# Performance work log

Measured on AMD Instinct MI355X. Metric: run time of the kernel, lower is better.

Reference implementation:

```python
import jax, jax.numpy as jnp
import numpy as np

N = 40000
E = 640000
DIN = 128
H = 128
G = 16
C = 10


def setup_inputs() -> dict:
    key = jax.random.key(0)
    ks = jax.random.split(key, 12)
    x = jax.random.normal(ks[0], (N, DIN), dtype=jnp.float32)
    edge_index = jax.random.randint(ks[1], (2, E), 0, N, dtype=jnp.int64)
    batch = jnp.sort(jax.random.randint(ks[2], (N,), 0, G, dtype=jnp.int64))
    s = 1.0 / np.sqrt(H)
    W_in = jax.random.normal(ks[3], (DIN, H), dtype=jnp.float32) * s
    b_in = jnp.zeros((H,), dtype=jnp.float32)
    W1 = jax.random.normal(ks[4], (H, H), dtype=jnp.float32) * s
    b1 = jnp.zeros((H,), dtype=jnp.float32)
    W2 = jax.random.normal(ks[5], (H, H), dtype=jnp.float32) * s
    b2 = jnp.zeros((H,), dtype=jnp.float32)
    Wf1 = jax.random.normal(ks[6], (H, H // 2), dtype=jnp.float32) * s
    bf1 = jnp.zeros((H // 2,), dtype=jnp.float32)
    Wf2 = jax.random.normal(ks[7], (H // 2, C), dtype=jnp.float32) * (1.0 / np.sqrt(H // 2))
    bf2 = jnp.zeros((C,), dtype=jnp.float32)
    return {"x": x, "edge_index": edge_index, "batch": batch,
            "W_in": W_in, "b_in": b_in, "W1": W1, "b1": b1,
            "W2": W2, "b2": b2, "Wf1": Wf1, "bf1": bf1,
            "Wf2": Wf2, "bf2": bf2}


def _gcn_conv(h, src, dst, deg_inv_sqrt, W, b):
    # h' = D^{-1/2} (A + I) D^{-1/2} (h W) + b  (PyG GCNConv with self-loops)
    hw = h @ W  # [N, H]
    norm = deg_inv_sqrt[src] * deg_inv_sqrt[dst]  # [E]
    agg = jax.ops.segment_sum(hw[src] * norm[:, None], dst, num_segments=N)
    agg = agg + hw * (deg_inv_sqrt * deg_inv_sqrt)[:, None]  # self-loop term
    return agg + b


def reference(x, edge_index, batch, W_in, b_in, W1, b1, W2, b2, Wf1, bf1, Wf2, bf2):
    src, dst = edge_index[0], edge_index[1]
    # degree on target nodes, including self-loop (+1)
    deg = jax.ops.segment_sum(jnp.ones((E,), dtype=x.dtype), dst, num_segments=N) + 1.0
    deg_inv_sqrt = jax.lax.rsqrt(deg)

    h = x @ W_in + b_in
    h = jax.nn.relu(_gcn_conv(h, src, dst, deg_inv_sqrt, W1, b1))  # dropout is identity in eval
    h = jax.nn.relu(_gcn_conv(h, src, dst, deg_inv_sqrt, W2, b2))

    # global mean pool by graph id
    sums = jax.ops.segment_sum(h, batch, num_segments=G)  # [G, H]
    counts = jax.ops.segment_sum(jnp.ones((N,), dtype=h.dtype), batch, num_segments=G)
    pooled = sums / jnp.maximum(counts, 1.0)[:, None]

    out = jax.nn.relu(pooled @ Wf1 + bf1) @ Wf2 + bf2  # [G, C]
    return out
```

## Files before the change

kernel.cpp:

```cpp
#include <hip/hip_runtime.h>

#define NN 40000
#define EE 640000
#define NCH 157

typedef unsigned int uint;
typedef unsigned short ushort;
typedef __attribute__((ext_vector_type(8))) short short8;
typedef __attribute__((ext_vector_type(4))) float floatx4;

__device__ inline ushort f2bf(float f) {
    uint u = __float_as_uint(f);
    return (ushort)((u + 0x7fffu + ((u >> 16) & 1u)) >> 16);
}
__device__ inline float bf_lo(uint u) { return __uint_as_float(u << 16); }
__device__ inline float bf_hi(uint u) { return __uint_as_float(u & 0xffff0000u); }

__device__ inline int lower_bound_dev(const int* __restrict__ a, int n, int x) {
    int lo = 0, hi = n;
    while (lo < hi) { int m = (lo + hi) >> 1; if (a[m] < x) lo = m + 1; else hi = m; }
    return lo;
}

__global__ __launch_bounds__(256) void histprep_kernel(const int* __restrict__ dst,
                                                       int* __restrict__ counts,
                                                       const float* __restrict__ W_in,
                                                       const float* __restrict__ W1,
                                                       const float* __restrict__ b_in,
                                                       const float* __restrict__ W2,
                                                       const int* __restrict__ batch,
                                                       ushort* __restrict__ Bp1,
                                                       ushort* __restrict__ Bp2,
                                                       float* __restrict__ cvec,
                                                       int* __restrict__ glo) {
    int b = blockIdx.x, t = threadIdx.x;
    if (b < 2500) {
        atomicAdd(&counts[dst[b * 256 + t]], 1);
    } else if (b < 2564) {
        int idx = (b - 2500) * 256 + t;
        int k = idx >> 7, n = idx & 127;
        float s = 0.f;
        for (int j = 0; j < 128; ++j) s = fmaf(W_in[k * 128 + j], W1[j * 128 + n], s);
        Bp1[((size_t)(k >> 3) * 128 + n) * 8 + (k & 7)] = f2bf(s);
    } else if (b < 2628) {
        int idx = (b - 2564) * 256 + t;
        int k = idx >> 7, n = idx & 127;
        Bp2[((size_t)(k >> 3) * 128 + n) * 8 + (k & 7)] = f2bf(W2[idx]);
    } else {
        if (t < 128) {
            float s = 0.f;
            for (int k = 0; k < 128; ++k) s = fmaf(b_in[k], W1[k * 128 + t], s);
            cvec[t] = s;
        } else if (t < 128 + 17) {
            int g = t - 128;
            glo[g] = lower_bound_dev(batch, NN, g);
        }
    }
}

__global__ __launch_bounds__(256) void scan_kernel(const int* __restrict__ counts,
                                                   int* __restrict__ goff,
                                                   int* __restrict__ start,
                                                   int* __restrict__ cursor,
                                                   float* __restrict__ dis, int N) {
    __shared__ int ws[4];
    __shared__ int sbase;
    int t = threadIdx.x, lane = t & 63, wv = t >> 6;
    int idx = blockIdx.x * 256 + t;
    int c = (idx < N) ? counts[idx] : 0;
    int v = c;
    #pragma unroll
    for (int d = 1; d < 64; d <<= 1) {
        int u = __shfl_up(v, d, 64);
        if (lane >= d) v += u;
    }
    if (lane == 63) ws[wv] = v;
    __syncthreads();
    if (t == 0) {
        int total = ws[0] + ws[1] + ws[2] + ws[3];
        sbase = atomicAdd(goff, total);
    }
    __syncthreads();
    int off = sbase;
    for (int j = 0; j < wv; ++j) off += ws[j];
    if (idx < N) {
        int excl = off + v - c;
        start[idx] = excl;
        cursor[idx] = excl;
        dis[idx] = rsqrtf((float)c + 1.0f);
    }
}

template <bool ABF16>
__device__ inline void mm_tile(const void* __restrict__ Av, const ushort* __restrict__ Bpack,
                               ushort* __restrict__ C, int tile, int wv, int lane) {
    int m = lane & 15, q = lane >> 4;
    int row = tile * 64 + wv * 16 + m;

    short8 afr[4];
    if (ABF16) {
        const ushort* A = (const ushort*)Av;
        const ushort* ap = A + (size_t)row * 128 + q * 8;
        #pragma unroll
        for (int k0 = 0; k0 < 4; ++k0) afr[k0] = *(const short8*)(ap + k0 * 32);
    } else {
        const float* A = (const float*)Av;
        const float* ap = A + (size_t)row * 128 + q * 8;
        #pragma unroll
        for (int k0 = 0; k0 < 4; ++k0) {
            float4 f0 = *(const float4*)(ap + k0 * 32);
            float4 f1 = *(const float4*)(ap + k0 * 32 + 4);
            short8 a;
            a[0] = (short)f2bf(f0.x); a[1] = (short)f2bf(f0.y);
            a[2] = (short)f2bf(f0.z); a[3] = (short)f2bf(f0.w);
            a[4] = (short)f2bf(f1.x); a[5] = (short)f2bf(f1.y);
            a[6] = (short)f2bf(f1.z); a[7] = (short)f2bf(f1.w);
            afr[k0] = a;
        }
    }

    floatx4 acc[8];
    #pragma unroll
    for (int nt = 0; nt < 8; ++nt) { floatx4 z = {0.f, 0.f, 0.f, 0.f}; acc[nt] = z; }

    #pragma unroll
    for (int nt = 0; nt < 8; ++nt) {
        #pragma unroll
        for (int k0 = 0; k0 < 4; ++k0) {
            short8 bfrag = *(const short8*)(Bpack + ((size_t)(k0 * 4 + q) * 128 + nt * 16 + m) * 8);
            acc[nt] = __builtin_amdgcn_mfma_f32_16x16x32_bf16(afr[k0], bfrag, acc[nt], 0, 0, 0);
        }
    }

    int orow_base = tile * 64 + wv * 16 + q * 4;
    #pragma unroll
    for (int nt = 0; nt < 8; ++nt) {
        #pragma unroll
        for (int r = 0; r < 4; ++r)
            C[(size_t)(orow_base + r) * 128 + nt * 16 + m] = f2bf(acc[nt][r]);
    }
}

__global__ __launch_bounds__(256) void fillmm1_kernel(const int* __restrict__ src,
                                                      const int* __restrict__ dst,
                                                      const float* __restrict__ dis,
                                                      int* __restrict__ cursor,
                                                      int2* __restrict__ edata,
                                                      const float* __restrict__ x,
                                                      const ushort* __restrict__ Bp1,
                                                      ushort* __restrict__ bufA) {
    int b = blockIdx.x, t = threadIdx.x;
    if (b < 2500) {
        int e = b * 256 + t;
        int s = src[e], d = dst[e];
        int pos = atomicAdd(&cursor[d], 1);
        float nrm = dis[s] * dis[d];
        int2 v; v.x = s; v.y = __float_as_int(nrm);
        edata[pos] = v;
    } else {
        mm_tile<false>(x, Bp1, bufA, b - 2500, t >> 6, t & 63);
    }
}

__global__ __launch_bounds__(256) void mm2_kernel(const ushort* __restrict__ A,
                                                  const ushort* __restrict__ Bp2,
                                                  ushort* __restrict__ C) {
    mm_tile<true>(A, Bp2, C, blockIdx.x, threadIdx.x >> 6, threadIdx.x & 63);
}

__global__ __launch_bounds__(256) void agg_kernel(const ushort* __restrict__ hw,
                                                  const float* __restrict__ dis,
                                                  const int* __restrict__ start,
                                                  const int* __restrict__ counts,
                                                  const int2* __restrict__ edata,
                                                  const float* __restrict__ cvec,
                                                  const float* __restrict__ bias,
                                                  ushort* __restrict__ out, int N) {
    __shared__ int2 eds[4][64];
    int wv = threadIdx.x >> 6;
    int lane = threadIdx.x & 63;
    int i = blockIdx.x * 4 + wv;
    if (i >= N) return;
    int beg = start[i];
    int deg = counts[i];
    int dmain = deg > 64 ? 64 : deg;
    const uint* __restrict__ hv = (const uint*)hw;

    int2 ed;
    if (lane < dmain) ed = edata[beg + lane];
    else { ed.x = i; ed.y = 0; }
    eds[wv][lane] = ed;

    float di = dis[i];
    float sii = di * di;
    uint su = hv[(size_t)i * 64 + lane];
    float a0 = sii * bf_lo(su);
    float a1 = sii * bf_hi(su);
    float sumnorm = sii;

    int dpad = (dmain + 7) & ~7;
    for (int j = 0; j < dpad; j += 8) {
        int2 e0 = eds[wv][j],     e1 = eds[wv][j + 1];
        int2 e2 = eds[wv][j + 2], e3 = eds[wv][j + 3];
        int2 e4 = eds[wv][j + 4], e5 = eds[wv][j + 5];
        int2 e6 = eds[wv][j + 6], e7 = eds[wv][j + 7];
        uint u0 = hv[(size_t)e0.x * 64 + lane];
        uint u1 = hv[(size_t)e1.x * 64 + lane];
        uint u2 = hv[(size_t)e2.x * 64 + lane];
        uint u3 = hv[(size_t)e3.x * 64 + lane];
        uint u4 = hv[(size_t)e4.x * 64 + lane];
        uint u5 = hv[(size_t)e5.x * 64 + lane];
        uint u6 = hv[(size_t)e6.x * 64 + lane];
        uint u7 = hv[(size_t)e7.x * 64 + lane];
        float n0 = __int_as_float(e0.y), n1 = __int_as_float(e1.y);
        float n2 = __int_as_float(e2.y), n3 = __int_as_float(e3.y);
        float n4 = __int_as_float(e4.y), n5 = __int_as_float(e5.y);
        float n6 = __int_as_float(e6.y), n7 = __int_as_float(e7.y);
        a0 = fmaf(n0, bf_lo(u0), a0); a1 = fmaf(n0, bf_hi(u0), a1);
        a0 = fmaf(n1, bf_lo(u1), a0); a1 = fmaf(n1, bf_hi(u1), a1);
        a0 = fmaf(n2, bf_lo(u2), a0); a1 = fmaf(n2, bf_hi(u2), a1);
        a0 = fmaf(n3, bf_lo(u3), a0); a1 = fmaf(n3, bf_hi(u3), a1);
        a0 = fmaf(n4, bf_lo(u4), a0); a1 = fmaf(n4, bf_hi(u4), a1);
        a0 = fmaf(n5, bf_lo(u5), a0); a1 = fmaf(n5, bf_hi(u5), a1);
        a0 = fmaf(n6, bf_lo(u6), a0); a1 = fmaf(n6, bf_hi(u6), a1);
        a0 = fmaf(n7, bf_lo(u7), a0); a1 = fmaf(n7, bf_hi(u7), a1);
        sumnorm += ((n0 + n1) + (n2 + n3)) + ((n4 + n5) + (n6 + n7));
    }
    for (int e = beg + 64; e < beg + deg; ++e) {
        int2 et = edata[e];
        float n0 = __int_as_float(et.y);
        uint u0 = hv[(size_t)et.x * 64 + lane];
        a0 = fmaf(n0, bf_lo(u0), a0);
        a1 = fmaf(n0, bf_hi(u0), a1);
        sumnorm += n0;
    }

    float c0 = 0.f, c1 = 0.f;
    if (cvec) { c0 = cvec[2 * lane]; c1 = cvec[2 * lane + 1]; }
    float b0 = bias[2 * lane], b1 = bias[2 * lane + 1];
    float o0 = fmaxf(fmaf(sumnorm, c0, a0) + b0, 0.f);
    float o1 = fmaxf(fmaf(sumnorm, c1, a1) + b1, 0.f);
    uint o = (uint)f2bf(o0) | ((uint)f2bf(o1) << 16);
    ((uint*)out)[(size_t)i * 64 + lane] = o;
}

__global__ __launch_bounds__(256) void poolfinal_kernel(const ushort* __restrict__ h,
                                                        const int* __restrict__ glo,
                                                        float* __restrict__ pools,
                                                        int* __restrict__ ticket,
                                                        const float* __restrict__ Wf1,
                                                        const float* __restrict__ bf1,
                                                        const float* __restrict__ Wf2,
                                                        const float* __restrict__ bf2,
                                                        float* __restrict__ out) {
    __shared__ float pooled[16][128];
    __shared__ float z[16][64];
    __shared__ int slast;
    int t = threadIdx.x, c2 = t & 63, wv = t >> 6;
    int b = blockIdx.x;
    int g = b >> 3, ch = b & 7;
    int lo = glo[g], hi = glo[g + 1];
    int span = hi - lo;
    int chunk = (span + 7) >> 3;
    int r0 = lo + ch * chunk;
    int r1 = hi < r0 + chunk ? hi : r0 + chunk;
    const uint* __restrict__ hv = (const uint*)h;

    float a0 = 0.f, a1 = 0.f;
    #pragma unroll 4
    for (int j = r0 + wv; j < r1; j += 4) {
        uint u = hv[(size_t)j * 64 + c2];
        a0 += bf_lo(u);
        a1 += bf_hi(u);
    }
    if (r0 < r1) {
        atomicAdd(&pools[g * 128 + 2 * c2], a0);
        atomicAdd(&pools[g * 128 + 2 * c2 + 1], a1);
    }

    __syncthreads();
    __threadfence();
    if (t == 0) slast = atomicAdd(ticket, 1);
    __syncthreads();
    if (slast != 127) return;

    for (int idx = t; idx < 2048; idx += 256) {
        int gg = idx >> 7, c = idx & 127;
        int cn = glo[gg + 1] - glo[gg];
        float cnf = (float)(cn > 1 ? cn : 1);
        float ps = __hip_atomic_load(&pools[idx], __ATOMIC_RELAXED, __HIP_MEMORY_SCOPE_AGENT);
        pooled[gg][c] = ps / cnf;
    }
    __syncthreads();
    for (int idx = t; idx < 1024; idx += 256) {
        int gg = idx >> 6, j = idx & 63;
        float s = bf1[j];
        for (int k = 0; k < 128; ++k) s = fmaf(pooled[gg][k], Wf1[k * 64 + j], s);
        z[gg][j] = fmaxf(s, 0.f);
    }
    __syncthreads();
    if (t < 160) {
        int gg = t / 10, k = t % 10;
        float s = bf2[k];
        for (int j = 0; j < 64; ++j) s = fmaf(z[gg][j], Wf2[j * 10 + k], s);
        out[t] = s;
    }
}


extern "C" void kernel_launch(void* const* d_in, const int* in_sizes, int n_in,
                              void* d_out, int out_size, void* d_ws, size_t ws_size,
                              hipStream_t stream) {
    const float* x    = (const float*)d_in[0];
    const int* edge   = (const int*)d_in[1];
    const int* batch  = (const int*)d_in[2];
    const float* W_in = (const float*)d_in[3];
    const float* b_in = (const float*)d_in[4];
    const float* W1   = (const float*)d_in[5];
    const float* b1   = (const float*)d_in[6];
    const float* W2   = (const float*)d_in[7];
    const float* b2   = (const float*)d_in[8];
    const float* Wf1  = (const float*)d_in[9];
    const float* bf1  = (const float*)d_in[10];
    const float* Wf2  = (const float*)d_in[11];
    const float* bf2  = (const float*)d_in[12];
    float* out = (float*)d_out;

    char* ws = (char*)d_ws;
    size_t off = 0;
    auto alloc = [&](size_t bytes) -> void* {
        void* p = ws + off;
        off += (bytes + 511) & ~(size_t)511;
        return p;
    };
    int* counts   = (int*)alloc((size_t)NN * 4);
    float* pools  = (float*)alloc(16 * 128 * 4);
    int* misc     = (int*)alloc(512);
    size_t zero_bytes = off;
    int* goff     = misc;
    int* ticket   = misc + 1;
    int* glo      = misc + 8;
    ushort* bufA  = (ushort*)alloc((size_t)NN * 128 * 2);
    ushort* bufB  = (ushort*)alloc((size_t)NN * 128 * 2);
    ushort* Bp1   = (ushort*)alloc(128 * 128 * 2);
    ushort* Bp2   = (ushort*)alloc(128 * 128 * 2);
    float* cvec   = (float*)alloc(128 * 4);
    float* dis    = (float*)alloc((size_t)NN * 4);
    int* start    = (int*)alloc((size_t)NN * 4);
    int* cursor   = (int*)alloc((size_t)NN * 4);
    int2* edata   = (int2*)alloc((size_t)EE * 8);

    hipMemsetAsync(counts, 0, zero_bytes, stream);

    histprep_kernel<<<2629, 256, 0, stream>>>(edge + EE, counts, W_in, W1, b_in, W2,
                                              batch, Bp1, Bp2, cvec, glo);
    scan_kernel<<<NCH, 256, 0, stream>>>(counts, goff, start, cursor, dis, NN);
    fillmm1_kernel<<<2500 + NN / 64, 256, 0, stream>>>(edge, edge + EE, dis, cursor,
                                                       edata, x, Bp1, bufA);
    agg_kernel<<<NN / 4, 256, 0, stream>>>(bufA, dis, start, counts, edata, cvec, b1, bufB, NN);
    mm2_kernel<<<NN / 64, 256, 0, stream>>>(bufB, Bp2, bufA);
    agg_kernel<<<NN / 4, 256, 0, stream>>>(bufA, dis, start, counts, edata, nullptr, b2, bufB, NN);
    poolfinal_kernel<<<128, 256, 0, stream>>>(bufB, glo, pools, ticket,
                                              Wf1, bf1, Wf2, bf2, out);
}
```

Measured before the change: 240.5 us.

## Fuse first aggregation with second matmul and second aggregation with mean pooling

The first GCN aggregation now writes a 16-row tile into shared memory, and the same block multiplies it by W2 with MFMA, so the separate mm2 launch and its round trip of h1 through global memory go away. The second aggregation accumulates the pooled sums directly, reducing per block in shared memory when all 16 rows belong to one graph and using atomics otherwise. The last block, found by a ticket counter, runs the final MLP. This removes two kernel launches and two full-size intermediate writes and reads. In exchange each aggregation block has only 4 waves processing 4 nodes each serially, and the matmul tile is smaller, which may lower occupancy and weight reuse.

```diff
diff --git a/kernel.cpp b/kernel.cpp
--- a/kernel.cpp
+++ b/kernel.cpp
@@ -91,32 +91,23 @@
     }
 }
 
-template <bool ABF16>
-__device__ inline void mm_tile(const void* __restrict__ Av, const ushort* __restrict__ Bpack,
-                               ushort* __restrict__ C, int tile, int wv, int lane) {
+__device__ inline void mm_tile_f32(const float* __restrict__ A, const ushort* __restrict__ Bpack,
+                                   ushort* __restrict__ C, int tile, int wv, int lane) {
     int m = lane & 15, q = lane >> 4;
     int row = tile * 64 + wv * 16 + m;
 
     short8 afr[4];
-    if (ABF16) {
-        const ushort* A = (const ushort*)Av;
-        const ushort* ap = A + (size_t)row * 128 + q * 8;
-        #pragma unroll
-        for (int k0 = 0; k0 < 4; ++k0) afr[k0] = *(const short8*)(ap + k0 * 32);
-    } else {
-        const float* A = (const float*)Av;
-        const float* ap = A + (size_t)row * 128 + q * 8;
-        #pragma unroll
-        for (int k0 = 0; k0 < 4; ++k0) {
-            float4 f0 = *(const float4*)(ap + k0 * 32);
-            float4 f1 = *(const float4*)(ap + k0 * 32 + 4);
-            short8 a;
-            a[0] = (short)f2bf(f0.x); a[1] = (short)f2bf(f0.y);
-            a[2] = (short)f2bf(f0.z); a[3] = (short)f2bf(f0.w);
-            a[4] = (short)f2bf(f1.x); a[5] = (short)f2bf(f1.y);
-            a[6] = (short)f2bf(f1.z); a[7] = (short)f2bf(f1.w);
-            afr[k0] = a;
-        }
+    const float* ap = A + (size_t)row * 128 + q * 8;
+    #pragma unroll
+    for (int k0 = 0; k0 < 4; ++k0) {
+        float4 f0 = *(const float4*)(ap + k0 * 32);
+        float4 f1 = *(const float4*)(ap + k0 * 32 + 4);
+        short8 a;
+        a[0] = (short)f2bf(f0.x); a[1] = (short)f2bf(f0.y);
+        a[2] = (short)f2bf(f0.z); a[3] = (short)f2bf(f0.w);
+        a[4] = (short)f2bf(f1.x); a[5] = (short)f2bf(f1.y);
+        a[6] = (short)f2bf(f1.z); a[7] = (short)f2bf(f1.w);
+        afr[k0] = a;
     }
 
     floatx4 acc[8];
@@ -158,38 +149,23 @@
         int2 v; v.x = s; v.y = __float_as_int(nrm);
         edata[pos] = v;
     } else {
-        mm_tile<false>(x, Bp1, bufA, b - 2500, t >> 6, t & 63);
-    }
-}
-
-__global__ __launch_bounds__(256) void mm2_kernel(const ushort* __restrict__ A,
-                                                  const ushort* __restrict__ Bp2,
-                                                  ushort* __restrict__ C) {
-    mm_tile<true>(A, Bp2, C, blockIdx.x, threadIdx.x >> 6, threadIdx.x & 63);
-}
-
-__global__ __launch_bounds__(256) void agg_kernel(const ushort* __restrict__ hw,
-                                                  const float* __restrict__ dis,
-                                                  const int* __restrict__ start,
-                                                  const int* __restrict__ counts,
-                                                  const int2* __restrict__ edata,
-                                                  const float* __restrict__ cvec,
-                                                  const float* __restrict__ bias,
-                                                  ushort* __restrict__ out, int N) {
-    __shared__ int2 eds[4][64];
-    int wv = threadIdx.x >> 6;
-    int lane = threadIdx.x & 63;
-    int i = blockIdx.x * 4 + wv;
-    if (i >= N) return;
+        mm_tile_f32(x, Bp1, bufA, b - 2500, t >> 6, t & 63);
+    }
+}
+
+__device__ inline void agg_core(const uint* __restrict__ hv, const float* __restrict__ dis,
+                                const int* __restrict__ start, const int* __restrict__ counts,
+                                const int2* __restrict__ edata, const float* __restrict__ cvec,
+                                const float* __restrict__ bias, int i, int lane,
+                                int2* __restrict__ eds, float& o0, float& o1) {
     int beg = start[i];
     int deg = counts[i];
     int dmain = deg > 64 ? 64 : deg;
-    const uint* __restrict__ hv = (const uint*)hw;
 
     int2 ed;
     if (lane < dmain) ed = edata[beg + lane];
     else { ed.x = i; ed.y = 0; }
-    eds[wv][lane] = ed;
+    eds[lane] = ed;
 
     float di = dis[i];
     float sii = di * di;
@@ -200,10 +176,10 @@
 
     int dpad = (dmain + 7) & ~7;
     for (int j = 0; j < dpad; j += 8) {
-        int2 e0 = eds[wv][j],     e1 = eds[wv][j + 1];
-        int2 e2 = eds[wv][j + 2], e3 = eds[wv][j + 3];
-        int2 e4 = eds[wv][j + 4], e5 = eds[wv][j + 5];
-        int2 e6 = eds[wv][j + 6], e7 = eds[wv][j + 7];
+        int2 e0 = eds[j],     e1 = eds[j + 1];
+        int2 e2 = eds[j + 2], e3 = eds[j + 3];
+        int2 e4 = eds[j + 4], e5 = eds[j + 5];
+        int2 e6 = eds[j + 6], e7 = eds[j + 7];
         uint u0 = hv[(size_t)e0.x * 64 + lane];
         uint u1 = hv[(size_t)e1.x * 64 + lane];
         uint u2 = hv[(size_t)e2.x * 64 + lane];
@@ -238,51 +214,119 @@
     float c0 = 0.f, c1 = 0.f;
     if (cvec) { c0 = cvec[2 * lane]; c1 = cvec[2 * lane + 1]; }
     float b0 = bias[2 * lane], b1 = bias[2 * lane + 1];
-    float o0 = fmaxf(fmaf(sumnorm, c0, a0) + b0, 0.f);
-    float o1 = fmaxf(fmaf(sumnorm, c1, a1) + b1, 0.f);
-    uint o = (uint)f2bf(o0) | ((uint)f2bf(o1) << 16);
-    ((uint*)out)[(size_t)i * 64 + lane] = o;
-}
-
-__global__ __launch_bounds__(256) void poolfinal_kernel(const ushort* __restrict__ h,
-                                                        const int* __restrict__ glo,
-                                                        float* __restrict__ pools,
-                                                        int* __restrict__ ticket,
-                                                        const float* __restrict__ Wf1,
-                                                        const float* __restrict__ bf1,
-                                                        const float* __restrict__ Wf2,
-                                                        const float* __restrict__ bf2,
-                                                        float* __restrict__ out) {
+    o0 = fmaxf(fmaf(sumnorm, c0, a0) + b0, 0.f);
+    o1 = fmaxf(fmaf(sumnorm, c1, a1) + b1, 0.f);
+}
+
+#define H1S 136
+__global__ __launch_bounds__(256) void aggmm2_kernel(const ushort* __restrict__ hw,
+                                                     const float* __restrict__ dis,
+                                                     const int* __restrict__ start,
+                                                     const int* __restrict__ counts,
+                                                     const int2* __restrict__ edata,
+                                                     const float* __restrict__ cvec,
+                                                     const float* __restrict__ b1,
+                                                     const ushort* __restrict__ Bp2,
+                                                     ushort* __restrict__ outHW) {
+    __shared__ ushort h1[16][H1S];
+    __shared__ int2 eds[4][64];
+    int t = threadIdx.x, w = t >> 6, lane = t & 63;
+    int tile = blockIdx.x;
+    const uint* hv = (const uint*)hw;
+
+    #pragma unroll 1
+    for (int s = 0; s < 4; ++s) {
+        int r = w * 4 + s;
+        int i = tile * 16 + r;
+        float o0, o1;
+        agg_core(hv, dis, start, counts, edata, cvec, b1, i, lane, eds[w], o0, o1);
+        uint o = (uint)f2bf(o0) | ((uint)f2bf(o1) << 16);
+        *(uint*)&h1[r][2 * lane] = o;
+    }
+    __syncthreads();
+
+    int m = lane & 15, q = lane >> 4;
+    short8 afr[4];
+    #pragma unroll
+    for (int k0 = 0; k0 < 4; ++k0)
+        afr[k0] = *(const short8*)&h1[m][k0 * 32 + q * 8];
+
+    floatx4 acc[2];
+    #pragma unroll
+    for (int n2 = 0; n2 < 2; ++n2) { floatx4 z = {0.f, 0.f, 0.f, 0.f}; acc[n2] = z; }
+    #pragma unroll
+    for (int n2 = 0; n2 < 2; ++n2) {
+        int nt = w * 2 + n2;
+        #pragma unroll
+        for (int k0 = 0; k0 < 4; ++k0) {
+            short8 bfrag = *(const short8*)(Bp2 + ((size_t)(k0 * 4 + q) * 128 + nt * 16 + m) * 8);
+            acc[n2] = __builtin_amdgcn_mfma_f32_16x16x32_bf16(afr[k0], bfrag, acc[n2], 0, 0, 0);
+        }
+    }
+    int orow = tile * 16 + q * 4;
+    #pragma unroll
+    for (int n2 = 0; n2 < 2; ++n2) {
+        #pragma unroll
+        for (int r = 0; r < 4; ++r)
+            outHW[(size_t)(orow + r) * 128 + (w * 2 + n2) * 16 + m] = f2bf(acc[n2][r]);
+    }
+}
+
+__global__ __launch_bounds__(256) void aggpool_kernel(const ushort* __restrict__ hw,
+                                                      const float* __restrict__ dis,
+                                                      const int* __restrict__ start,
+                                                      const int* __restrict__ counts,
+                                                      const int2* __restrict__ edata,
+                                                      const float* __restrict__ b2,
+                                                      const int* __restrict__ batch,
+                                                      const int* __restrict__ glo,
+                                                      float* __restrict__ pools,
+                                                      int* __restrict__ ticket,
+                                                      const float* __restrict__ Wf1,
+                                                      const float* __restrict__ bf1,
+                                                      const float* __restrict__ Wf2,
+                                                      const float* __restrict__ bf2,
+                                                      float* __restrict__ out) {
+    __shared__ int2 eds[4][64];
+    __shared__ float wpool[4][128];
+    __shared__ int slast;
     __shared__ float pooled[16][128];
     __shared__ float z[16][64];
-    __shared__ int slast;
-    int t = threadIdx.x, c2 = t & 63, wv = t >> 6;
-    int b = blockIdx.x;
-    int g = b >> 3, ch = b & 7;
-    int lo = glo[g], hi = glo[g + 1];
-    int span = hi - lo;
-    int chunk = (span + 7) >> 3;
-    int r0 = lo + ch * chunk;
-    int r1 = hi < r0 + chunk ? hi : r0 + chunk;
-    const uint* __restrict__ hv = (const uint*)h;
-
-    float a0 = 0.f, a1 = 0.f;
-    #pragma unroll 4
-    for (int j = r0 + wv; j < r1; j += 4) {
-        uint u = hv[(size_t)j * 64 + c2];
-        a0 += bf_lo(u);
-        a1 += bf_hi(u);
-    }
-    if (r0 < r1) {
-        atomicAdd(&pools[g * 128 + 2 * c2], a0);
-        atomicAdd(&pools[g * 128 + 2 * c2 + 1], a1);
+    int t = threadIdx.x, w = t >> 6, lane = t & 63;
+    int tile = blockIdx.x;
+    const uint* hv = (const uint*)hw;
+
+    int gfirst = batch[tile * 16];
+    bool uni = (gfirst == batch[tile * 16 + 15]);
+
+    float p0 = 0.f, p1 = 0.f;
+    #pragma unroll 1
+    for (int s = 0; s < 4; ++s) {
+        int i = tile * 16 + w * 4 + s;
+        float o0, o1;
+        agg_core(hv, dis, start, counts, edata, nullptr, b2, i, lane, eds[w], o0, o1);
+        if (uni) { p0 += o0; p1 += o1; }
+        else {
+            int g = batch[i];
+            atomicAdd(&pools[g * 128 + 2 * lane], o0);
+            atomicAdd(&pools[g * 128 + 2 * lane + 1], o1);
+        }
+    }
+    if (uni) {
+        wpool[w][2 * lane] = p0;
+        wpool[w][2 * lane + 1] = p1;
+    }
+    __syncthreads();
+    if (uni && t < 128) {
+        float s = wpool[0][t] + wpool[1][t] + wpool[2][t] + wpool[3][t];
+        atomicAdd(&pools[gfirst * 128 + t], s);
     }
 
     __syncthreads();
     __threadfence();
     if (t == 0) slast = atomicAdd(ticket, 1);
     __syncthreads();
-    if (slast != 127) return;
+    if (slast != 2499) return;
 
     for (int idx = t; idx < 2048; idx += 256) {
         int gg = idx >> 7, c = idx & 127;
@@ -357,9 +401,9 @@
     scan_kernel<<<NCH, 256, 0, stream>>>(counts, goff, start, cursor, dis, NN);
     fillmm1_kernel<<<2500 + NN / 64, 256, 0, stream>>>(edge, edge + EE, dis, cursor,
                                                        edata, x, Bp1, bufA);
-    agg_kernel<<<NN / 4, 256, 0, stream>>>(bufA, dis, start, counts, edata, cvec, b1, bufB, NN);
-    mm2_kernel<<<NN / 64, 256, 0, stream>>>(bufB, Bp2, bufA);
-    agg_kernel<<<NN / 4, 256, 0, stream>>>(bufA, dis, start, counts, edata, nullptr, b2, bufB, NN);
-    poolfinal_kernel<<<128, 256, 0, stream>>>(bufB, glo, pools, ticket,
-                                              Wf1, bf1, Wf2, bf2, out);
-}
+    aggmm2_kernel<<<NN / 16, 256, 0, stream>>>(bufA, dis, start, counts, edata,
+                                               cvec, b1, Bp2, bufB);
+    aggpool_kernel<<<NN / 16, 256, 0, stream>>>(bufB, dis, start, counts, edata,
+                                                b2, batch, glo, pools, ticket,
+                                                Wf1, bf1, Wf2, bf2, out);
+}
```

Result: slower. 408.6 us (+69.9%).
